# Performance work log

Measured on AMD Instinct MI355X. Metric: run time of the kernel, lower is better.

Reference implementation:

```python
import jax, jax.numpy as jnp
import numpy as np
import math

B, H, N, D = 2, 16, 2048, 64

def setup_inputs() -> dict:
    key = jax.random.key(0)
    kq, kk, kv, kb = jax.random.split(key, 4)
    return {
        "query": jax.random.normal(kq, (B, H, N, D), dtype=jnp.float32),
        "key": jax.random.normal(kk, (B, H, N, D), dtype=jnp.float32),
        "value": jax.random.normal(kv, (B, H, N, D), dtype=jnp.float32),
        "relative_position_bias": jax.random.normal(kb, (H, N, N), dtype=jnp.float32),
    }

def reference(query, key, value, relative_position_bias):
    d = query.shape[-1]
    # scores: [B,H,N,N]
    attn = jnp.einsum("bhnd,bhmd->bhnm", query, key) / jnp.sqrt(jnp.asarray(d, query.dtype))
    attn = attn + relative_position_bias[None]  # broadcast over batch
    attn = jax.nn.softmax(attn, axis=-1)
    # dropout p=0.0 -> identity
    output = jnp.einsum("bhnm,bhmd->bhnd", attn, value)
    return (output, attn)
```

## Files before the change

### kernel.cpp

```cpp
#include <hip/hip_runtime.h>
#include <cstdint>

#define BN 2
#define HN 16
#define NN 2048
#define DD 64
#define KT 64
#define NT (NN / KT)
#define LDP 72
#define LDH 36

typedef __attribute__((ext_vector_type(8))) short short8;
typedef __attribute__((ext_vector_type(2))) uint32_t uint2v;
typedef __attribute__((ext_vector_type(4))) uint32_t uint4v;
typedef __attribute__((ext_vector_type(4))) float float4v;

static __device__ __forceinline__ uint32_t cvt_pk_bf16(float a, float b){
    uint32_t r;
    asm("v_cvt_pk_bf16_f32 %0, %1, %2" : "=v"(r) : "v"(a), "v"(b));
    return r;
}
static __device__ __forceinline__ unsigned short f2bf1(float a){
    return (unsigned short)(cvt_pk_bf16(a, a) & 0xffffu);
}
static __device__ __forceinline__ short8 pack8(float4v f0, float4v f1){
    uint4v u;
    u[0] = cvt_pk_bf16(f0[0], f0[1]);
    u[1] = cvt_pk_bf16(f0[2], f0[3]);
    u[2] = cvt_pk_bf16(f1[0], f1[1]);
    u[3] = cvt_pk_bf16(f1[2], f1[3]);
    return __builtin_bit_cast(short8, u);
}

static __device__ __forceinline__ float4v mfma_bf16(short8 a, short8 b, float4v c){
    return __builtin_amdgcn_mfma_f32_16x16x32_bf16(a, b, c, 0, 0, 0);
}

static __device__ __forceinline__ void barrier_lds(){
    asm volatile("s_waitcnt lgkmcnt(0)" ::: "memory");
    __builtin_amdgcn_s_barrier();
    asm volatile("" ::: "memory");
}

__launch_bounds__(256, 4)
__global__ void attn_fused_kernel(const float* __restrict__ Q,
                                  const float* __restrict__ K,
                                  const float* __restrict__ V,
                                  const float* __restrict__ Bias,
                                  float* __restrict__ Out){
    __shared__ unsigned short Kb[KT][LDP];
    __shared__ unsigned short Vt[DD][LDP];
    __shared__ uint32_t Pbh[4][16][LDH];

    const int raw  = blockIdx.x;
    const int slot = raw & 7;
    const int idx  = raw >> 3;
    const int b    = idx & 1;
    const int ghr  = slot * 64 + (idx >> 1);
    const int h    = ghr >> 5;
    const int rt   = ghr & 31;

    const int tid = threadIdx.x;
    const int l   = tid & 63;
    const int w   = tid >> 6;
    const int lg  = l >> 4;
    const int ll  = l & 15;
    const int vc  = ll * 4;

    const int srow = tid >> 4;
    const int scol = (tid & 15) << 2;
    const int vsw  = ((tid >> 1) & 7) << 3;

    const int qw = rt * 64 + w * 16;
    const size_t bh = (size_t)(b * HN + h);
    const float* Qg = Q + (bh * NN + qw) * DD;
    const float* Kg = K + bh * NN * DD;
    const float* Vg = V + bh * NN * DD;
    const float* BgA = Bias + (size_t)h * NN * NN + (size_t)(qw + lg * 4) * NN + ll;

    short8 qf[2];
    {
        const float* qrow = Qg + (size_t)ll * DD + lg * 8;
        #pragma unroll
        for(int ks = 0; ks < 2; ++ks)
            qf[ks] = pack8(*(const float4v*)(qrow + ks * 32),
                           *(const float4v*)(qrow + ks * 32 + 4));
    }

    float lsum[4];
    #pragma unroll
    for(int r = 0; r < 4; ++r) lsum[r] = 0.f;

    float4v kreg[4];
    #pragma unroll
    for(int i = 0; i < 4; ++i)
        kreg[i] = *(const float4v*)(Kg + (size_t)(srow + 16*i) * DD + scol);

    for(int ct = 0; ct < NT; ++ct){
        barrier_lds();
        #pragma unroll
        for(int i = 0; i < 4; ++i){
            uint2v t = { cvt_pk_bf16(kreg[i][0], kreg[i][1]),
                         cvt_pk_bf16(kreg[i][2], kreg[i][3]) };
            *(uint2v*)&Kb[srow + 16*i][scol] = t;
        }
        float bb[16];
        #pragma unroll
        for(int sub = 0; sub < 4; ++sub)
            #pragma unroll
            for(int r = 0; r < 4; ++r)
                bb[sub*4+r] = BgA[(size_t)r * NN + ct*KT + sub*16];
        if(ct + 1 < NT){
            #pragma unroll
            for(int i = 0; i < 4; ++i)
                kreg[i] = *(const float4v*)(Kg + (size_t)((ct+1)*KT + srow + 16*i) * DD + scol);
        }
        barrier_lds();

        float4v acc[4];
        #pragma unroll
        for(int sub = 0; sub < 4; ++sub) acc[sub] = (float4v){0.f,0.f,0.f,0.f};
        __builtin_amdgcn_s_setprio(1);
        #pragma unroll
        for(int sub = 0; sub < 4; ++sub){
            short8 b0 = *(const short8*)&Kb[sub*16 + ll][lg*8];
            short8 b1 = *(const short8*)&Kb[sub*16 + ll][32 + lg*8];
            acc[sub] = mfma_bf16(qf[0], b0, acc[sub]);
            acc[sub] = mfma_bf16(qf[1], b1, acc[sub]);
        }
        __builtin_amdgcn_s_setprio(0);

        #pragma unroll
        for(int r = 0; r < 4; ++r){
            float e0 = __expf(acc[0][r] * 0.125f + bb[r]);
            float e1 = __expf(acc[1][r] * 0.125f + bb[4+r]);
            float e2 = __expf(acc[2][r] * 0.125f + bb[8+r]);
            float e3 = __expf(acc[3][r] * 0.125f + bb[12+r]);
            lsum[r] += (e0 + e1) + (e2 + e3);
        }
    }

    float rl[4];
    #pragma unroll
    for(int r = 0; r < 4; ++r){
        #pragma unroll
        for(int d = 1; d < 16; d <<= 1) lsum[r] += __shfl_xor(lsum[r], d);
        rl[r] = 1.0f / lsum[r];
    }

    float4v oacc[4];
    #pragma unroll
    for(int ds = 0; ds < 4; ++ds) oacc[ds] = (float4v){0.f,0.f,0.f,0.f};

    float* attnW = Out + (size_t)BN*HN*NN*DD
                 + (bh * NN + qw + lg) * (size_t)NN + vc;

    float4v vreg[4];
    #pragma unroll
    for(int i = 0; i < 4; ++i){
        kreg[i] = *(const float4v*)(Kg + (size_t)(srow + 16*i) * DD + scol);
        vreg[i] = *(const float4v*)(Vg + (size_t)(srow + 16*i) * DD + scol);
    }

    for(int ct = 0; ct < NT; ++ct){
        barrier_lds();
        #pragma unroll
        for(int i = 0; i < 4; ++i){
            uint2v t = { cvt_pk_bf16(kreg[i][0], kreg[i][1]),
                         cvt_pk_bf16(kreg[i][2], kreg[i][3]) };
            *(uint2v*)&Kb[srow + 16*i][scol] = t;
            #pragma unroll
            for(int j = 0; j < 4; ++j)
                Vt[scol + j][(srow + 16*i) ^ vsw] = f2bf1(vreg[i][j]);
        }
        float bb[16];
        #pragma unroll
        for(int sub = 0; sub < 4; ++sub)
            #pragma unroll
            for(int r = 0; r < 4; ++r)
                bb[sub*4+r] = BgA[(size_t)r * NN + ct*KT + sub*16];
        if(ct + 1 < NT){
            #pragma unroll
            for(int i = 0; i < 4; ++i){
                kreg[i] = *(const float4v*)(Kg + (size_t)((ct+1)*KT + srow + 16*i) * DD + scol);
                vreg[i] = *(const float4v*)(Vg + (size_t)((ct+1)*KT + srow + 16*i) * DD + scol);
            }
        }
        barrier_lds();

        float4v acc[4];
        #pragma unroll
        for(int sub = 0; sub < 4; ++sub) acc[sub] = (float4v){0.f,0.f,0.f,0.f};
        __builtin_amdgcn_s_setprio(1);
        #pragma unroll
        for(int sub = 0; sub < 4; ++sub){
            short8 b0 = *(const short8*)&Kb[sub*16 + ll][lg*8];
            short8 b1 = *(const short8*)&Kb[sub*16 + ll][32 + lg*8];
            acc[sub] = mfma_bf16(qf[0], b0, acc[sub]);
            acc[sub] = mfma_bf16(qf[1], b1, acc[sub]);
        }
        __builtin_amdgcn_s_setprio(0);

        #pragma unroll
        for(int sub = 0; sub < 4; ++sub)
            #pragma unroll
            for(int r = 0; r < 4; ++r){
                float p = __expf(acc[sub][r] * 0.125f + bb[sub*4+r]) * rl[r];
                ((unsigned short*)&Pbh[w][lg*4 + r][0])[sub*16 + ll] = f2bf1(p);
            }

        asm volatile("s_waitcnt lgkmcnt(0)" ::: "memory");

        short8 pf0 = __builtin_bit_cast(short8, *(const uint4v*)&Pbh[w][ll][lg*4]);
        short8 pf1 = __builtin_bit_cast(short8, *(const uint4v*)&Pbh[w][ll][16 + lg*4]);

        #pragma unroll
        for(int it = 0; it < 4; ++it){
            uint2v pw = *(const uint2v*)&Pbh[w][lg + 4*it][ll*2];
            float4v pv;
            pv[0] = __builtin_bit_cast(float, pw[0] << 16);
            pv[1] = __builtin_bit_cast(float, pw[0] & 0xffff0000u);
            pv[2] = __builtin_bit_cast(float, pw[1] << 16);
            pv[3] = __builtin_bit_cast(float, pw[1] & 0xffff0000u);
            *(float4v*)(attnW + (size_t)(it*4) * NN + ct*KT) = pv;
        }

        __builtin_amdgcn_s_setprio(1);
        #pragma unroll
        for(int ds = 0; ds < 4; ++ds){
            const int rsw = (2*ds + (ll >> 3)) << 3;
            short8 v0 = *(const short8*)&Vt[ds*16 + ll][(lg*8) ^ rsw];
            short8 v1 = *(const short8*)&Vt[ds*16 + ll][(32 + lg*8) ^ rsw];
            oacc[ds] = mfma_bf16(pf0, v0, oacc[ds]);
            oacc[ds] = mfma_bf16(pf1, v1, oacc[ds]);
        }
        __builtin_amdgcn_s_setprio(0);
    }

    float* outG = Out + (bh * NN + qw) * (size_t)DD;
    #pragma unroll
    for(int ds = 0; ds < 4; ++ds)
        #pragma unroll
        for(int r = 0; r < 4; ++r)
            outG[(size_t)(lg*4 + r) * DD + ds*16 + ll] = oacc[ds][r];
}

extern "C" void kernel_launch(void* const* d_in, const int* in_sizes, int n_in,
                              void* d_out, int out_size, void* d_ws, size_t ws_size,
                              hipStream_t stream) {
    const float* q    = (const float*)d_in[0];
    const float* k    = (const float*)d_in[1];
    const float* v    = (const float*)d_in[2];
    const float* bias = (const float*)d_in[3];
    float* out = (float*)d_out;

    dim3 grid(BN * HN * (NN / 64));
    dim3 block(256);
    hipLaunchKernelGGL(attn_fused_kernel, grid, block, 0, stream, q, k, v, bias, out);
}
```

Measured before the change: 355.9 us.

## Load bias as coalesced float4 rows and compute softmax in row layout

Bias is now read as float4 vectors along rows instead of scattered scalar loads in the MFMA output layout. To match, raw scaled scores are staged through an fp32 LDS buffer and transposed into row layout, where the exp, sum and normalization happen. The stored attention probabilities become full fp32 rather than bf16-rounded values, which also changes the output precision. The cost is extra LDS traffic (fp32 scores written and read twice per tile, plus a larger shared buffer) and additional waitcnt drains.

```diff
diff --git a/kernel.cpp b/kernel.cpp
--- a/kernel.cpp
+++ b/kernel.cpp
@@ -8,7 +8,7 @@
 #define KT 64
 #define NT (NN / KT)
 #define LDP 72
-#define LDH 36
+#define LDF 68
 
 typedef __attribute__((ext_vector_type(8))) short short8;
 typedef __attribute__((ext_vector_type(2))) uint32_t uint2v;
@@ -40,6 +40,9 @@
     asm volatile("s_waitcnt lgkmcnt(0)" ::: "memory");
     __builtin_amdgcn_s_barrier();
     asm volatile("" ::: "memory");
+}
+static __device__ __forceinline__ void lgkm_drain(){
+    asm volatile("s_waitcnt lgkmcnt(0)" ::: "memory");
 }
 
 __launch_bounds__(256, 4)
@@ -50,7 +53,7 @@
                                   float* __restrict__ Out){
     __shared__ unsigned short Kb[KT][LDP];
     __shared__ unsigned short Vt[DD][LDP];
-    __shared__ uint32_t Pbh[4][16][LDH];
+    __shared__ float Pb[4][16][LDF];
 
     const int raw  = blockIdx.x;
     const int slot = raw & 7;
@@ -76,7 +79,7 @@
     const float* Qg = Q + (bh * NN + qw) * DD;
     const float* Kg = K + bh * NN * DD;
     const float* Vg = V + bh * NN * DD;
-    const float* BgA = Bias + (size_t)h * NN * NN + (size_t)(qw + lg * 4) * NN + ll;
+    const float* BgV = Bias + (size_t)h * NN * NN + (size_t)(qw + lg) * NN + vc;
 
     short8 qf[2];
     {
@@ -87,9 +90,9 @@
                            *(const float4v*)(qrow + ks * 32 + 4));
     }
 
-    float lsum[4];
-    #pragma unroll
-    for(int r = 0; r < 4; ++r) lsum[r] = 0.f;
+    float lsumv[4];
+    #pragma unroll
+    for(int it = 0; it < 4; ++it) lsumv[it] = 0.f;
 
     float4v kreg[4];
     #pragma unroll
@@ -98,18 +101,16 @@
 
     for(int ct = 0; ct < NT; ++ct){
         barrier_lds();
+        float4v bv[4];
+        #pragma unroll
+        for(int it = 0; it < 4; ++it)
+            bv[it] = *(const float4v*)(BgV + (size_t)(it * 4) * NN + ct*KT);
         #pragma unroll
         for(int i = 0; i < 4; ++i){
             uint2v t = { cvt_pk_bf16(kreg[i][0], kreg[i][1]),
                          cvt_pk_bf16(kreg[i][2], kreg[i][3]) };
             *(uint2v*)&Kb[srow + 16*i][scol] = t;
         }
-        float bb[16];
-        #pragma unroll
-        for(int sub = 0; sub < 4; ++sub)
-            #pragma unroll
-            for(int r = 0; r < 4; ++r)
-                bb[sub*4+r] = BgA[(size_t)r * NN + ct*KT + sub*16];
         if(ct + 1 < NT){
             #pragma unroll
             for(int i = 0; i < 4; ++i)
@@ -131,21 +132,26 @@
         __builtin_amdgcn_s_setprio(0);
 
         #pragma unroll
-        for(int r = 0; r < 4; ++r){
-            float e0 = __expf(acc[0][r] * 0.125f + bb[r]);
-            float e1 = __expf(acc[1][r] * 0.125f + bb[4+r]);
-            float e2 = __expf(acc[2][r] * 0.125f + bb[8+r]);
-            float e3 = __expf(acc[3][r] * 0.125f + bb[12+r]);
-            lsum[r] += (e0 + e1) + (e2 + e3);
-        }
-    }
-
-    float rl[4];
-    #pragma unroll
-    for(int r = 0; r < 4; ++r){
-        #pragma unroll
-        for(int d = 1; d < 16; d <<= 1) lsum[r] += __shfl_xor(lsum[r], d);
-        rl[r] = 1.0f / lsum[r];
+        for(int sub = 0; sub < 4; ++sub)
+            #pragma unroll
+            for(int r = 0; r < 4; ++r)
+                Pb[w][lg*4 + r][sub*16 + ll] = acc[sub][r] * 0.125f;
+        lgkm_drain();
+
+        #pragma unroll
+        for(int it = 0; it < 4; ++it){
+            float4v sv = *(const float4v*)&Pb[w][it*4 + lg][vc];
+            lsumv[it] += (__expf(sv[0] + bv[it][0]) + __expf(sv[1] + bv[it][1]))
+                       + (__expf(sv[2] + bv[it][2]) + __expf(sv[3] + bv[it][3]));
+        }
+    }
+
+    float rlv[4];
+    #pragma unroll
+    for(int it = 0; it < 4; ++it){
+        #pragma unroll
+        for(int d = 1; d < 16; d <<= 1) lsumv[it] += __shfl_xor(lsumv[it], d);
+        rlv[it] = 1.0f / lsumv[it];
     }
 
     float4v oacc[4];
@@ -164,6 +170,10 @@
 
     for(int ct = 0; ct < NT; ++ct){
         barrier_lds();
+        float4v bv[4];
+        #pragma unroll
+        for(int it = 0; it < 4; ++it)
+            bv[it] = *(const float4v*)(BgV + (size_t)(it * 4) * NN + ct*KT);
         #pragma unroll
         for(int i = 0; i < 4; ++i){
             uint2v t = { cvt_pk_bf16(kreg[i][0], kreg[i][1]),
@@ -173,12 +183,6 @@
             for(int j = 0; j < 4; ++j)
                 Vt[scol + j][(srow + 16*i) ^ vsw] = f2bf1(vreg[i][j]);
         }
-        float bb[16];
-        #pragma unroll
-        for(int sub = 0; sub < 4; ++sub)
-            #pragma unroll
-            for(int r = 0; r < 4; ++r)
-                bb[sub*4+r] = BgA[(size_t)r * NN + ct*KT + sub*16];
         if(ct + 1 < NT){
             #pragma unroll
             for(int i = 0; i < 4; ++i){
@@ -204,25 +208,31 @@
         #pragma unroll
         for(int sub = 0; sub < 4; ++sub)
             #pragma unroll
-            for(int r = 0; r < 4; ++r){
-                float p = __expf(acc[sub][r] * 0.125f + bb[sub*4+r]) * rl[r];
-                ((unsigned short*)&Pbh[w][lg*4 + r][0])[sub*16 + ll] = f2bf1(p);
-            }
-
-        asm volatile("s_waitcnt lgkmcnt(0)" ::: "memory");
-
-        short8 pf0 = __builtin_bit_cast(short8, *(const uint4v*)&Pbh[w][ll][lg*4]);
-        short8 pf1 = __builtin_bit_cast(short8, *(const uint4v*)&Pbh[w][ll][16 + lg*4]);
+            for(int r = 0; r < 4; ++r)
+                Pb[w][lg*4 + r][sub*16 + ll] = acc[sub][r] * 0.125f;
+        lgkm_drain();
 
         #pragma unroll
         for(int it = 0; it < 4; ++it){
-            uint2v pw = *(const uint2v*)&Pbh[w][lg + 4*it][ll*2];
-            float4v pv;
-            pv[0] = __builtin_bit_cast(float, pw[0] << 16);
-            pv[1] = __builtin_bit_cast(float, pw[0] & 0xffff0000u);
-            pv[2] = __builtin_bit_cast(float, pw[1] << 16);
-            pv[3] = __builtin_bit_cast(float, pw[1] & 0xffff0000u);
-            *(float4v*)(attnW + (size_t)(it*4) * NN + ct*KT) = pv;
+            float4v sv = *(const float4v*)&Pb[w][it*4 + lg][vc];
+            float4v p;
+            p[0] = __expf(sv[0] + bv[it][0]) * rlv[it];
+            p[1] = __expf(sv[1] + bv[it][1]) * rlv[it];
+            p[2] = __expf(sv[2] + bv[it][2]) * rlv[it];
+            p[3] = __expf(sv[3] + bv[it][3]) * rlv[it];
+            *(float4v*)(attnW + (size_t)(it*4) * NN + ct*KT) = p;
+            *(float4v*)&Pb[w][it*4 + lg][vc] = p;
+        }
+        lgkm_drain();
+
+        short8 pf0, pf1;
+        {
+            float4v p0 = *(const float4v*)&Pb[w][ll][lg*8];
+            float4v p1 = *(const float4v*)&Pb[w][ll][lg*8 + 4];
+            float4v p2 = *(const float4v*)&Pb[w][ll][32 + lg*8];
+            float4v p3 = *(const float4v*)&Pb[w][ll][32 + lg*8 + 4];
+            pf0 = pack8(p0, p1);
+            pf1 = pack8(p2, p3);
         }
 
         __builtin_amdgcn_s_setprio(1);
```

Result: no change. 350.0 us (-1.6%).
